# Kernel optimization log

Hardware: AMD Instinct MI355X
Metric: run time of the kernel (lower is better)

The kernel has to match this reference:

```python
import jax, jax.numpy as jnp
import numpy as np

EPS = 1e-07

def setup_inputs() -> dict:
    key = jax.random.key(0)
    foreground = jax.random.normal(key, (8, 256, 64, 64), dtype=jnp.float32)
    return {"foreground": foreground}

def reference(foreground):
    bs, ch, h, w = foreground.shape
    # kernels: one 1x1 kernel per spatial position, L2-normalized over channels
    K = foreground.reshape(bs, ch, h * w).transpose(0, 2, 1) + EPS      # [b, hw, c]
    K = K / jnp.sqrt(jnp.sum(K * K, axis=2, keepdims=True))
    # conv2d with 1x1 kernels == per-pixel dot product against every kernel.
    # (padding=patch_size//2 in the torch code is exactly cancelled by the
    #  matching padding of the conv_transpose2d, so it is omitted.)
    scores = jnp.einsum('bkc,bchw->bkhw', K, foreground)                # [b, hw, h, w]
    attn = jax.nn.softmax(scores, axis=1)
    # conv_transpose2d with the same 1x1 kernels == K^T @ attn per pixel
    out = jnp.einsum('bkc,bkhw->bchw', K, attn)                         # [b, c, h, w]
    return out
```

## Files before the change

kernel.cpp:

```cpp
#include <hip/hip_runtime.h>


#define BATCH 8
#define CH 256
#define NPIX 4096
#define EPSV 1e-7f
#define L2E 1.4426950408889634f

using bf16x8 = __attribute__((ext_vector_type(8))) __bf16;
using bf16x4 = __attribute__((ext_vector_type(4))) __bf16;
using f32x4  = __attribute__((ext_vector_type(4))) float;

__device__ __forceinline__ void gload16(const void* g, void* l) {
  __builtin_amdgcn_global_load_lds(
      (const __attribute__((address_space(1))) unsigned int*)g,
      (__attribute__((address_space(3))) unsigned int*)l, 16, 0, 0);
}

__device__ __forceinline__ void barrier_full() {
  asm volatile("s_waitcnt vmcnt(0) lgkmcnt(0)\n"
               "s_barrier" ::: "memory");
}
__device__ __forceinline__ void barrier_lgkm() {
  asm volatile("s_waitcnt lgkmcnt(0)\n"
               "s_barrier" ::: "memory");
}

__global__ __launch_bounds__(256)
void ca_prep(const float* __restrict__ F, __bf16* __restrict__ KA,
             __bf16* __restrict__ KB) {
  const int b   = blockIdx.x;
  const int kt  = blockIdx.y;
  const int kt0 = kt * 32;
  const int t   = threadIdx.x;
  const int k   = t & 31;
  const int h   = (t >> 5) & 1;
  const int w   = t >> 6;

  const float* __restrict__ Fb = F + (size_t)b * CH * NPIX;

  __shared__ float red[4][32];
  __shared__ float invk[32];
  __shared__ __align__(16) __bf16 T[32][264];

  float fv[32];
  float ss = 0.f;
#pragma unroll
  for (int rep = 0; rep < 32; ++rep) {
    int c = rep * 8 + w * 2 + h;
    float v = Fb[(size_t)c * NPIX + kt0 + k] + EPSV;
    fv[rep] = v;
    ss = fmaf(v, v, ss);
  }
  ss += __shfl_xor(ss, 32, 64);
  if ((t & 32) == 0) red[w][k] = ss;
  __syncthreads();
  if (t < 32) invk[t] = rsqrtf(red[0][t] + red[1][t] + red[2][t] + red[3][t]);
  __syncthreads();
  const float iv = invk[k];
#pragma unroll
  for (int rep = 0; rep < 32; ++rep) {
    int c = rep * 8 + w * 2 + h;
    T[k][c] = (__bf16)(fv[rep] * iv);
  }
  __syncthreads();

  __bf16* KAp = KA + ((size_t)b * 128 + kt) * (32 * 256);
#pragma unroll
  for (int pass = 0; pass < 4; ++pass) {
    int kk = pass * 8 + (t >> 5);
    int u  = t & 31;
    bf16x8 v = *(const bf16x8*)&T[kk][u * 8];
    *(bf16x8*)&KAp[kk * 256 + ((u ^ (kk & 7)) * 8)] = v;
  }
  __bf16* KBp = KB + ((size_t)b * 128 + kt) * (256 * 32);
#pragma unroll
  for (int pass = 0; pass < 4; ++pass) {
    int c = pass * 64 + (t >> 2);
    int v = t & 3;
    bf16x8 o;
#pragma unroll
    for (int j = 0; j < 8; ++j) o[j] = T[v * 8 + j][c];
    *(bf16x8*)&KBp[c * 32 + v * 8] = o;
  }
}

__global__ __launch_bounds__(1024, 4)
void ca_attn9(const float* __restrict__ F, const __bf16* __restrict__ KA,
              const __bf16* __restrict__ KB, float* __restrict__ Out) {
  __shared__ __align__(16) char smem[98304];

  const int tid  = threadIdx.x;
  const int lane = tid & 63;
  const int w    = tid >> 6;
  const int lq   = lane & 15;
  const int lg   = lane >> 4;
  const int b    = blockIdx.x;
  const int q0   = blockIdx.y * 128;

  const char* KAb = (const char*)(KA + (size_t)b * (size_t)NPIX * CH);
  const char* KBb = (const char*)(KB + (size_t)b * (size_t)NPIX * CH);
  char* PlB = smem + 65536;

  if (w < 8) {
    const int kh = w >> 2, qh = w & 3;
    const int qA = q0 + qh * 32 + lq;
    const int qB = qA + 16;
    const float* __restrict__ Fb = F + (size_t)b * CH * NPIX;
    const int wo = w * 4096;

#pragma unroll
    for (int j = 0; j < 4; ++j)
      gload16(KAb + wo + j * 1024 + lane * 16, smem + wo + j * 1024);

    bf16x8 qfA[8], qfB[8];
    float ssA = 0.f, ssB = 0.f;
#pragma unroll
    for (int cf = 0; cf < 8; ++cf) {
#pragma unroll
      for (int j = 0; j < 8; ++j) {
        int c = cf * 32 + lg * 8 + j;
        float va = Fb[(size_t)c * NPIX + qA];
        float vb = Fb[(size_t)c * NPIX + qB];
        qfA[cf][j] = (__bf16)(va * L2E);
        qfB[cf][j] = (__bf16)(vb * L2E);
        ssA = fmaf(va, va, ssA);
        ssB = fmaf(vb, vb, ssB);
      }
    }
    ssA += __shfl_xor(ssA, 16, 64); ssA += __shfl_xor(ssA, 32, 64);
    ssB += __shfl_xor(ssB, 16, 64); ssB += __shfl_xor(ssB, 32, 64);
    const float mqA = sqrtf(ssA) * L2E, mqB = sqrtf(ssB) * L2E;

    float lA = 0.f, lB = 0.f;
    const int krow = kh * 16 + lq;
    const int ksw  = lq & 7;
    const int rowByte = krow * 512;
    const int pwRowA = (qh * 32 + lq) * 128;
    const int pwRowB = pwRowA + 16 * 128;
    const int puBase = kh * 2 + (lg >> 1);
    const int pwSub  = ((lg & 1) << 3);
    const int u0 = (puBase ^ ksw) << 4;
    const int u1 = ((4 + puBase) ^ ksw) << 4;

    barrier_full();

    const f32x4 zero = {0.f, 0.f, 0.f, 0.f};
    for (int i = 0; i < 64; ++i) {
      const int cb = i & 1;
      if (i < 63) {
        const char* s = KAb + (size_t)(i + 1) * 32768;
        char* d = smem + (cb ^ 1) * 32768;
#pragma unroll
        for (int j = 0; j < 4; ++j)
          gload16(s + wo + j * 1024 + lane * 16, d + wo + j * 1024);
      }

      const char* ab0 = smem + cb * 32768 + rowByte;
      const char* ab1 = ab0 + 16384;
      f32x4 s00 = zero, s01 = zero, s10 = zero, s11 = zero;
      __builtin_amdgcn_s_setprio(1);
#pragma unroll
      for (int cf = 0; cf < 8; ++cf) {
        const int uo = ((((cf << 2) | lg) ^ ksw) << 4);
        bf16x8 a0 = *(const bf16x8*)(ab0 + uo);
        bf16x8 a1 = *(const bf16x8*)(ab1 + uo);
        s00 = __builtin_amdgcn_mfma_f32_16x16x32_bf16(a0, qfA[cf], s00, 0, 0, 0);
        s01 = __builtin_amdgcn_mfma_f32_16x16x32_bf16(a0, qfB[cf], s01, 0, 0, 0);
        s10 = __builtin_amdgcn_mfma_f32_16x16x32_bf16(a1, qfA[cf], s10, 0, 0, 0);
        s11 = __builtin_amdgcn_mfma_f32_16x16x32_bf16(a1, qfB[cf], s11, 0, 0, 0);
      }
      __builtin_amdgcn_s_setprio(0);

      char* pb = PlB + cb * 16384;
      bf16x4 pv00, pv01, pv10, pv11;
#pragma unroll
      for (int r = 0; r < 4; ++r) {
        float p00 = __builtin_amdgcn_exp2f(s00[r] - mqA);
        float p01 = __builtin_amdgcn_exp2f(s01[r] - mqB);
        float p10 = __builtin_amdgcn_exp2f(s10[r] - mqA);
        float p11 = __builtin_amdgcn_exp2f(s11[r] - mqB);
        lA += p00 + p10; lB += p01 + p11;
        pv00[r] = (__bf16)p00; pv01[r] = (__bf16)p01;
        pv10[r] = (__bf16)p10; pv11[r] = (__bf16)p11;
      }
      *(bf16x4*)(pb + pwRowA + u0 + pwSub) = pv00;
      *(bf16x4*)(pb + pwRowB + u0 + pwSub) = pv01;
      *(bf16x4*)(pb + pwRowA + u1 + pwSub) = pv10;
      *(bf16x4*)(pb + pwRowB + u1 + pwSub) = pv11;

      barrier_full();
    }

    lA += __shfl_xor(lA, 16, 64); lA += __shfl_xor(lA, 32, 64);
    lB += __shfl_xor(lB, 16, 64); lB += __shfl_xor(lB, 32, 64);
    float* lE = (float*)smem;
    if (lg == 0) lE[kh * 128 + qh * 32 + lq] = lA;
    if (lg == 1) lE[kh * 128 + qh * 32 + 16 + lq] = lB;
    barrier_full();

  } else {
    const int cq  = w - 8;
    const int c0  = (cq >> 1) * 64;
    const int qh2 = cq & 1;
    const size_t fragBase = (size_t)(c0 + lq) * 64 + (size_t)lg * 16;
    const int prRow = (qh2 * 64 + lq) * 128;
    const int prU0  = ((0 * 4 + lg) ^ (lq & 7)) << 4;
    const int prU1  = ((1 * 4 + lg) ^ (lq & 7)) << 4;

    const f32x4 zero = {0.f, 0.f, 0.f, 0.f};
    f32x4 oacc[4][4];
#pragma unroll
    for (int i = 0; i < 4; ++i)
#pragma unroll
      for (int j = 0; j < 4; ++j) oacc[i][j] = zero;

    barrier_lgkm();

    for (int jt = 0; jt < 64; ++jt) {
      const char* kb0 = KBb + (size_t)(2 * jt) * 16384 + fragBase;
      const char* kb1 = kb0 + 16384;
      bf16x8 k00 = *(const bf16x8*)(kb0);
      bf16x8 k01 = *(const bf16x8*)(kb0 + 1024);
      bf16x8 k02 = *(const bf16x8*)(kb0 + 2048);
      bf16x8 k03 = *(const bf16x8*)(kb0 + 3072);
      bf16x8 k10 = *(const bf16x8*)(kb1);
      bf16x8 k11 = *(const bf16x8*)(kb1 + 1024);
      bf16x8 k12 = *(const bf16x8*)(kb1 + 2048);
      bf16x8 k13 = *(const bf16x8*)(kb1 + 3072);

      barrier_lgkm();

      const char* pb = PlB + (jt & 1) * 16384;
      __builtin_amdgcn_s_setprio(1);
#pragma unroll
      for (int qf = 0; qf < 4; ++qf) {
        bf16x8 pf0 = *(const bf16x8*)(pb + prRow + qf * 2048 + prU0);
        oacc[0][qf] = __builtin_amdgcn_mfma_f32_16x16x32_bf16(k00, pf0, oacc[0][qf], 0, 0, 0);
        oacc[1][qf] = __builtin_amdgcn_mfma_f32_16x16x32_bf16(k01, pf0, oacc[1][qf], 0, 0, 0);
        oacc[2][qf] = __builtin_amdgcn_mfma_f32_16x16x32_bf16(k02, pf0, oacc[2][qf], 0, 0, 0);
        oacc[3][qf] = __builtin_amdgcn_mfma_f32_16x16x32_bf16(k03, pf0, oacc[3][qf], 0, 0, 0);
      }
#pragma unroll
      for (int qf = 0; qf < 4; ++qf) {
        bf16x8 pf1 = *(const bf16x8*)(pb + prRow + qf * 2048 + prU1);
        oacc[0][qf] = __builtin_amdgcn_mfma_f32_16x16x32_bf16(k10, pf1, oacc[0][qf], 0, 0, 0);
        oacc[1][qf] = __builtin_amdgcn_mfma_f32_16x16x32_bf16(k11, pf1, oacc[1][qf], 0, 0, 0);
        oacc[2][qf] = __builtin_amdgcn_mfma_f32_16x16x32_bf16(k12, pf1, oacc[2][qf], 0, 0, 0);
        oacc[3][qf] = __builtin_amdgcn_mfma_f32_16x16x32_bf16(k13, pf1, oacc[3][qf], 0, 0, 0);
      }
      __builtin_amdgcn_s_setprio(0);
    }

    barrier_lgkm();

    const float* lE = (const float*)smem;
    const int qb = qh2 * 64;
    float rl0 = 1.0f / (lE[qb + 0 * 16 + lq] + lE[128 + qb + 0 * 16 + lq]);
    float rl1 = 1.0f / (lE[qb + 1 * 16 + lq] + lE[128 + qb + 1 * 16 + lq]);
    float rl2 = 1.0f / (lE[qb + 2 * 16 + lq] + lE[128 + qb + 2 * 16 + lq]);
    float rl3 = 1.0f / (lE[qb + 3 * 16 + lq] + lE[128 + qb + 3 * 16 + lq]);
    float* __restrict__ Ob = Out + (size_t)b * CH * NPIX;
#pragma unroll
    for (int ct = 0; ct < 4; ++ct) {
#pragma unroll
      for (int r = 0; r < 4; ++r) {
        const int c = c0 + ct * 16 + lg * 4 + r;
        float* orow = Ob + (size_t)c * NPIX + q0 + qb;
        orow[0 * 16 + lq] = oacc[ct][0][r] * rl0;
        orow[1 * 16 + lq] = oacc[ct][1][r] * rl1;
        orow[2 * 16 + lq] = oacc[ct][2][r] * rl2;
        orow[3 * 16 + lq] = oacc[ct][3][r] * rl3;
      }
    }
  }
}

extern "C" void kernel_launch(void* const* d_in, const int* in_sizes, int n_in,
                              void* d_out, int out_size, void* d_ws, size_t ws_size,
                              hipStream_t stream) {
  const float* F = (const float*)d_in[0];
  float* out = (float*)d_out;
  const size_t imgElems = (size_t)BATCH * NPIX * CH;

  __bf16* KAi = (__bf16*)d_ws;
  __bf16* KBi = KAi + imgElems;
  ca_prep<<<dim3(BATCH, 128), 256, 0, stream>>>(F, KAi, KBi);
  ca_attn9<<<dim3(BATCH, 32), 1024, 0, stream>>>(F, KAi, KBi, out);
}
```

Before: 133.1 us.

## Switch PV consumer waves to 32x32x16 MFMA with matching KB layout

The consumer waves that accumulate K^T·P now use 32x32x16 bf16 MFMAs on 32x32 output tiles instead of 16x16x32 MFMAs on 16x16 tiles. The prep kernel writes KB in a new chunked layout so each lane's operand fragment is one contiguous 16-byte load. This cuts the number of MFMA issues and P-fragment LDS reads per iteration. The producer waves also keep raised priority through the softmax and P store, which may favour them over the consumer waves.

```diff
diff --git a/kernel.cpp b/kernel.cpp
--- a/kernel.cpp
+++ b/kernel.cpp
@@ -10,6 +10,7 @@
 using bf16x8 = __attribute__((ext_vector_type(8))) __bf16;
 using bf16x4 = __attribute__((ext_vector_type(4))) __bf16;
 using f32x4  = __attribute__((ext_vector_type(4))) float;
+using f32x16 = __attribute__((ext_vector_type(16))) float;
 
 __device__ __forceinline__ void gload16(const void* g, void* l) {
   __builtin_amdgcn_global_load_lds(
@@ -73,21 +74,26 @@
     bf16x8 v = *(const bf16x8*)&T[kk][u * 8];
     *(bf16x8*)&KAp[kk * 256 + ((u ^ (kk & 7)) * 8)] = v;
   }
-  __bf16* KBp = KB + ((size_t)b * 128 + kt) * (256 * 32);
-#pragma unroll
-  for (int pass = 0; pass < 4; ++pass) {
-    int c = pass * 64 + (t >> 2);
-    int v = t & 3;
-    bf16x8 o;
-#pragma unroll
-    for (int j = 0; j < 8; ++j) o[j] = T[v * 8 + j][c];
-    *(bf16x8*)&KBp[c * 32 + v * 8] = o;
+  {
+    const int jt = kt >> 1;
+    char* KBp = (char*)KB + ((size_t)b * 64 + jt) * 32768;
+#pragma unroll
+    for (int pass = 0; pass < 4; ++pass) {
+      int c  = pass * 64 + (t >> 2);
+      int v  = t & 3;
+      int kc = (kt & 1) * 2 + (v >> 1);
+      int hi = v & 1;
+      bf16x8 o;
+#pragma unroll
+      for (int j = 0; j < 8; ++j) o[j] = T[v * 8 + j][c];
+      *(bf16x8*)(KBp + kc * 8192 + c * 32 + hi * 16) = o;
+    }
   }
 }
 
 __global__ __launch_bounds__(1024, 4)
-void ca_attn9(const float* __restrict__ F, const __bf16* __restrict__ KA,
-              const __bf16* __restrict__ KB, float* __restrict__ Out) {
+void ca_attn10(const float* __restrict__ F, const __bf16* __restrict__ KA,
+               const __bf16* __restrict__ KB, float* __restrict__ Out) {
   __shared__ __align__(16) char smem[98304];
 
   const int tid  = threadIdx.x;
@@ -156,10 +162,11 @@
           gload16(s + wo + j * 1024 + lane * 16, d + wo + j * 1024);
       }
 
+      __builtin_amdgcn_s_setprio(1);
+
       const char* ab0 = smem + cb * 32768 + rowByte;
       const char* ab1 = ab0 + 16384;
       f32x4 s00 = zero, s01 = zero, s10 = zero, s11 = zero;
-      __builtin_amdgcn_s_setprio(1);
 #pragma unroll
       for (int cf = 0; cf < 8; ++cf) {
         const int uo = ((((cf << 2) | lg) ^ ksw) << 4);
@@ -170,7 +177,6 @@
         s10 = __builtin_amdgcn_mfma_f32_16x16x32_bf16(a1, qfA[cf], s10, 0, 0, 0);
         s11 = __builtin_amdgcn_mfma_f32_16x16x32_bf16(a1, qfB[cf], s11, 0, 0, 0);
       }
-      __builtin_amdgcn_s_setprio(0);
 
       char* pb = PlB + cb * 16384;
       bf16x4 pv00, pv01, pv10, pv11;
@@ -188,6 +194,7 @@
       *(bf16x4*)(pb + pwRowB + u0 + pwSub) = pv01;
       *(bf16x4*)(pb + pwRowA + u1 + pwSub) = pv10;
       *(bf16x4*)(pb + pwRowB + u1 + pwSub) = pv11;
+      __builtin_amdgcn_s_setprio(0);
 
       barrier_full();
     }
@@ -203,75 +210,62 @@
     const int cq  = w - 8;
     const int c0  = (cq >> 1) * 64;
     const int qh2 = cq & 1;
-    const size_t fragBase = (size_t)(c0 + lq) * 64 + (size_t)lg * 16;
-    const int prRow = (qh2 * 64 + lq) * 128;
-    const int prU0  = ((0 * 4 + lg) ^ (lq & 7)) << 4;
-    const int prU1  = ((1 * 4 + lg) ^ (lq & 7)) << 4;
-
-    const f32x4 zero = {0.f, 0.f, 0.f, 0.f};
-    f32x4 oacc[4][4];
-#pragma unroll
-    for (int i = 0; i < 4; ++i)
-#pragma unroll
-      for (int j = 0; j < 4; ++j) oacc[i][j] = zero;
+    const int l31 = lane & 31;
+    const int hi  = lane >> 5;
+    const size_t cBase = (size_t)(c0 + l31) * 32 + (size_t)hi * 16;
+    const int q7 = l31 & 7;
+    const int prRow0 = (qh2 * 64 + l31) * 128;
+    const int prRow1 = prRow0 + 32 * 128;
+
+    f32x16 o00 = (f32x16)0.0f, o01 = (f32x16)0.0f;
+    f32x16 o10 = (f32x16)0.0f, o11 = (f32x16)0.0f;
 
     barrier_lgkm();
 
     for (int jt = 0; jt < 64; ++jt) {
-      const char* kb0 = KBb + (size_t)(2 * jt) * 16384 + fragBase;
-      const char* kb1 = kb0 + 16384;
-      bf16x8 k00 = *(const bf16x8*)(kb0);
-      bf16x8 k01 = *(const bf16x8*)(kb0 + 1024);
-      bf16x8 k02 = *(const bf16x8*)(kb0 + 2048);
-      bf16x8 k03 = *(const bf16x8*)(kb0 + 3072);
-      bf16x8 k10 = *(const bf16x8*)(kb1);
-      bf16x8 k11 = *(const bf16x8*)(kb1 + 1024);
-      bf16x8 k12 = *(const bf16x8*)(kb1 + 2048);
-      bf16x8 k13 = *(const bf16x8*)(kb1 + 3072);
+      const char* kcb = KBb + (size_t)jt * 32768;
+      bf16x8 a00 = *(const bf16x8*)(kcb + 0 * 8192 + cBase);
+      bf16x8 a01 = *(const bf16x8*)(kcb + 1 * 8192 + cBase);
+      bf16x8 a02 = *(const bf16x8*)(kcb + 2 * 8192 + cBase);
+      bf16x8 a03 = *(const bf16x8*)(kcb + 3 * 8192 + cBase);
+      bf16x8 a10 = *(const bf16x8*)(kcb + 0 * 8192 + cBase + 1024);
+      bf16x8 a11 = *(const bf16x8*)(kcb + 1 * 8192 + cBase + 1024);
+      bf16x8 a12 = *(const bf16x8*)(kcb + 2 * 8192 + cBase + 1024);
+      bf16x8 a13 = *(const bf16x8*)(kcb + 3 * 8192 + cBase + 1024);
 
       barrier_lgkm();
 
       const char* pb = PlB + (jt & 1) * 16384;
-      __builtin_amdgcn_s_setprio(1);
-#pragma unroll
-      for (int qf = 0; qf < 4; ++qf) {
-        bf16x8 pf0 = *(const bf16x8*)(pb + prRow + qf * 2048 + prU0);
-        oacc[0][qf] = __builtin_amdgcn_mfma_f32_16x16x32_bf16(k00, pf0, oacc[0][qf], 0, 0, 0);
-        oacc[1][qf] = __builtin_amdgcn_mfma_f32_16x16x32_bf16(k01, pf0, oacc[1][qf], 0, 0, 0);
-        oacc[2][qf] = __builtin_amdgcn_mfma_f32_16x16x32_bf16(k02, pf0, oacc[2][qf], 0, 0, 0);
-        oacc[3][qf] = __builtin_amdgcn_mfma_f32_16x16x32_bf16(k03, pf0, oacc[3][qf], 0, 0, 0);
-      }
-#pragma unroll
-      for (int qf = 0; qf < 4; ++qf) {
-        bf16x8 pf1 = *(const bf16x8*)(pb + prRow + qf * 2048 + prU1);
-        oacc[0][qf] = __builtin_amdgcn_mfma_f32_16x16x32_bf16(k10, pf1, oacc[0][qf], 0, 0, 0);
-        oacc[1][qf] = __builtin_amdgcn_mfma_f32_16x16x32_bf16(k11, pf1, oacc[1][qf], 0, 0, 0);
-        oacc[2][qf] = __builtin_amdgcn_mfma_f32_16x16x32_bf16(k12, pf1, oacc[2][qf], 0, 0, 0);
-        oacc[3][qf] = __builtin_amdgcn_mfma_f32_16x16x32_bf16(k13, pf1, oacc[3][qf], 0, 0, 0);
-      }
-      __builtin_amdgcn_s_setprio(0);
+#pragma unroll
+      for (int kc = 0; kc < 4; ++kc) {
+        const int uo = (((kc << 1) | hi) ^ q7) << 4;
+        bf16x8 p0 = *(const bf16x8*)(pb + prRow0 + uo);
+        bf16x8 p1 = *(const bf16x8*)(pb + prRow1 + uo);
+        bf16x8 a0 = kc == 0 ? a00 : kc == 1 ? a01 : kc == 2 ? a02 : a03;
+        bf16x8 a1 = kc == 0 ? a10 : kc == 1 ? a11 : kc == 2 ? a12 : a13;
+        o00 = __builtin_amdgcn_mfma_f32_32x32x16_bf16(a0, p0, o00, 0, 0, 0);
+        o01 = __builtin_amdgcn_mfma_f32_32x32x16_bf16(a0, p1, o01, 0, 0, 0);
+        o10 = __builtin_amdgcn_mfma_f32_32x32x16_bf16(a1, p0, o10, 0, 0, 0);
+        o11 = __builtin_amdgcn_mfma_f32_32x32x16_bf16(a1, p1, o11, 0, 0, 0);
+      }
     }
 
     barrier_lgkm();
 
     const float* lE = (const float*)smem;
     const int qb = qh2 * 64;
-    float rl0 = 1.0f / (lE[qb + 0 * 16 + lq] + lE[128 + qb + 0 * 16 + lq]);
-    float rl1 = 1.0f / (lE[qb + 1 * 16 + lq] + lE[128 + qb + 1 * 16 + lq]);
-    float rl2 = 1.0f / (lE[qb + 2 * 16 + lq] + lE[128 + qb + 2 * 16 + lq]);
-    float rl3 = 1.0f / (lE[qb + 3 * 16 + lq] + lE[128 + qb + 3 * 16 + lq]);
+    const float rl0 = 1.0f / (lE[qb + l31] + lE[128 + qb + l31]);
+    const float rl1 = 1.0f / (lE[qb + 32 + l31] + lE[128 + qb + 32 + l31]);
     float* __restrict__ Ob = Out + (size_t)b * CH * NPIX;
 #pragma unroll
-    for (int ct = 0; ct < 4; ++ct) {
-#pragma unroll
-      for (int r = 0; r < 4; ++r) {
-        const int c = c0 + ct * 16 + lg * 4 + r;
-        float* orow = Ob + (size_t)c * NPIX + q0 + qb;
-        orow[0 * 16 + lq] = oacc[ct][0][r] * rl0;
-        orow[1 * 16 + lq] = oacc[ct][1][r] * rl1;
-        orow[2 * 16 + lq] = oacc[ct][2][r] * rl2;
-        orow[3 * 16 + lq] = oacc[ct][3][r] * rl3;
-      }
+    for (int r = 0; r < 16; ++r) {
+      const int crow = (r & 3) + 8 * (r >> 2) + 4 * hi;
+      float* orow0 = Ob + (size_t)(c0 + crow) * NPIX + q0 + qb;
+      float* orow1 = Ob + (size_t)(c0 + 32 + crow) * NPIX + q0 + qb;
+      orow0[l31]      = o00[r] * rl0;
+      orow0[32 + l31] = o01[r] * rl1;
+      orow1[l31]      = o10[r] * rl0;
+      orow1[32 + l31] = o11[r] * rl1;
     }
   }
 }
@@ -286,5 +280,5 @@
   __bf16* KAi = (__bf16*)d_ws;
   __bf16* KBi = KAi + imgElems;
   ca_prep<<<dim3(BATCH, 128), 256, 0, stream>>>(F, KAi, KBi);
-  ca_attn9<<<dim3(BATCH, 32), 1024, 0, stream>>>(F, KAi, KBi, out);
-}
+  ca_attn10<<<dim3(BATCH, 32), 1024, 0, stream>>>(F, KAi, KBi, out);
+}
```

New measurement: 139.6 us. 4.9% more time.

## Store key tiles in MFMA fragment order and load them directly from global

Applied to the files above, without the earlier changes.

The prep kernel now writes the normalized key matrix in a fragment-ordered layout, so each lane's 16-byte MFMA operand sits at a contiguous, coalesced address. The score-producing waves then read key fragments straight from global/L2 into registers, replacing the double-buffered global_load_lds staging through a 64 KB LDS region. This cuts LDS use to the probability buffers, which may allow more blocks per CU, and removes the vmcnt waits from the barriers. In exchange, the score MFMAs depend on global-load latency inside the loop, with no explicit prefetch to hide it.

```diff
diff --git a/kernel.cpp b/kernel.cpp
--- a/kernel.cpp
+++ b/kernel.cpp
@@ -11,23 +11,13 @@
 using bf16x4 = __attribute__((ext_vector_type(4))) __bf16;
 using f32x4  = __attribute__((ext_vector_type(4))) float;
 
-__device__ __forceinline__ void gload16(const void* g, void* l) {
-  __builtin_amdgcn_global_load_lds(
-      (const __attribute__((address_space(1))) unsigned int*)g,
-      (__attribute__((address_space(3))) unsigned int*)l, 16, 0, 0);
-}
-
-__device__ __forceinline__ void barrier_full() {
-  asm volatile("s_waitcnt vmcnt(0) lgkmcnt(0)\n"
-               "s_barrier" ::: "memory");
-}
 __device__ __forceinline__ void barrier_lgkm() {
   asm volatile("s_waitcnt lgkmcnt(0)\n"
                "s_barrier" ::: "memory");
 }
 
 __global__ __launch_bounds__(256)
-void ca_prep(const float* __restrict__ F, __bf16* __restrict__ KA,
+void ca_prep(const float* __restrict__ F, __bf16* __restrict__ KAF,
              __bf16* __restrict__ KB) {
   const int b   = blockIdx.x;
   const int kt  = blockIdx.y;
@@ -65,30 +55,38 @@
   }
   __syncthreads();
 
-  __bf16* KAp = KA + ((size_t)b * 128 + kt) * (32 * 256);
-#pragma unroll
-  for (int pass = 0; pass < 4; ++pass) {
-    int kk = pass * 8 + (t >> 5);
-    int u  = t & 31;
-    bf16x8 v = *(const bf16x8*)&T[kk][u * 8];
-    *(bf16x8*)&KAp[kk * 256 + ((u ^ (kk & 7)) * 8)] = v;
-  }
-  __bf16* KBp = KB + ((size_t)b * 128 + kt) * (256 * 32);
-#pragma unroll
-  for (int pass = 0; pass < 4; ++pass) {
-    int c = pass * 64 + (t >> 2);
-    int v = t & 3;
-    bf16x8 o;
-#pragma unroll
-    for (int j = 0; j < 8; ++j) o[j] = T[v * 8 + j][c];
-    *(bf16x8*)&KBp[c * 32 + v * 8] = o;
+  {
+    const int jt = kt >> 1, st = kt & 1;
+    char* KAFp = (char*)KAF + ((size_t)b * 64 + jt) * 32768 + st * 16384;
+#pragma unroll
+    for (int pass = 0; pass < 4; ++pass) {
+      int slot = pass * 256 + t;
+      int cf   = slot >> 7;
+      int krow = (slot >> 2) & 31;
+      int lgi  = slot & 3;
+      bf16x8 v = *(const bf16x8*)&T[krow][cf * 32 + lgi * 8];
+      *(bf16x8*)(KAFp + slot * 16) = v;
+    }
+  }
+  {
+    __bf16* KBp = KB + ((size_t)b * 128 + kt) * (256 * 32);
+#pragma unroll
+    for (int pass = 0; pass < 4; ++pass) {
+      int c = pass * 64 + (t >> 2);
+      int v = t & 3;
+      bf16x8 o;
+#pragma unroll
+      for (int j = 0; j < 8; ++j) o[j] = T[v * 8 + j][c];
+      *(bf16x8*)&KBp[c * 32 + v * 8] = o;
+    }
   }
 }
 
 __global__ __launch_bounds__(1024, 4)
-void ca_attn9(const float* __restrict__ F, const __bf16* __restrict__ KA,
-              const __bf16* __restrict__ KB, float* __restrict__ Out) {
-  __shared__ __align__(16) char smem[98304];
+void ca_attn11(const float* __restrict__ F, const __bf16* __restrict__ KAF,
+               const __bf16* __restrict__ KB, float* __restrict__ Out) {
+  __shared__ __align__(16) char Pl[2][16384];
+  __shared__ float lE[256];
 
   const int tid  = threadIdx.x;
   const int lane = tid & 63;
@@ -98,20 +96,14 @@
   const int b    = blockIdx.x;
   const int q0   = blockIdx.y * 128;
 
-  const char* KAb = (const char*)(KA + (size_t)b * (size_t)NPIX * CH);
-  const char* KBb = (const char*)(KB + (size_t)b * (size_t)NPIX * CH);
-  char* PlB = smem + 65536;
+  const char* KFb = (const char*)KAF + (size_t)b * (size_t)NPIX * CH * 2;
+  const char* KBb = (const char*)KB + (size_t)b * (size_t)NPIX * CH * 2;
 
   if (w < 8) {
     const int kh = w >> 2, qh = w & 3;
     const int qA = q0 + qh * 32 + lq;
     const int qB = qA + 16;
     const float* __restrict__ Fb = F + (size_t)b * CH * NPIX;
-    const int wo = w * 4096;
-
-#pragma unroll
-    for (int j = 0; j < 4; ++j)
-      gload16(KAb + wo + j * 1024 + lane * 16, smem + wo + j * 1024);
 
     bf16x8 qfA[8], qfB[8];
     float ssA = 0.f, ssB = 0.f;
@@ -133,9 +125,8 @@
     const float mqA = sqrtf(ssA) * L2E, mqB = sqrtf(ssB) * L2E;
 
     float lA = 0.f, lB = 0.f;
-    const int krow = kh * 16 + lq;
-    const int ksw  = lq & 7;
-    const int rowByte = krow * 512;
+    const int ksw = lq & 7;
+    const char* abase0 = KFb + kh * 1024 + lq * 64 + lg * 16;
     const int pwRowA = (qh * 32 + lq) * 128;
     const int pwRowB = pwRowA + 16 * 128;
     const int puBase = kh * 2 + (lg >> 1);
@@ -143,28 +134,19 @@
     const int u0 = (puBase ^ ksw) << 4;
     const int u1 = ((4 + puBase) ^ ksw) << 4;
 
-    barrier_full();
+    barrier_lgkm();
 
     const f32x4 zero = {0.f, 0.f, 0.f, 0.f};
     for (int i = 0; i < 64; ++i) {
       const int cb = i & 1;
-      if (i < 63) {
-        const char* s = KAb + (size_t)(i + 1) * 32768;
-        char* d = smem + (cb ^ 1) * 32768;
-#pragma unroll
-        for (int j = 0; j < 4; ++j)
-          gload16(s + wo + j * 1024 + lane * 16, d + wo + j * 1024);
-      }
-
-      const char* ab0 = smem + cb * 32768 + rowByte;
-      const char* ab1 = ab0 + 16384;
+      const char* ab = abase0 + (size_t)i * 32768;
+
       f32x4 s00 = zero, s01 = zero, s10 = zero, s11 = zero;
       __builtin_amdgcn_s_setprio(1);
 #pragma unroll
       for (int cf = 0; cf < 8; ++cf) {
-        const int uo = ((((cf << 2) | lg) ^ ksw) << 4);
-        bf16x8 a0 = *(const bf16x8*)(ab0 + uo);
-        bf16x8 a1 = *(const bf16x8*)(ab1 + uo);
+        bf16x8 a0 = *(const bf16x8*)(ab + cf * 2048);
+        bf16x8 a1 = *(const bf16x8*)(ab + 16384 + cf * 2048);
         s00 = __builtin_amdgcn_mfma_f32_16x16x32_bf16(a0, qfA[cf], s00, 0, 0, 0);
         s01 = __builtin_amdgcn_mfma_f32_16x16x32_bf16(a0, qfB[cf], s01, 0, 0, 0);
         s10 = __builtin_amdgcn_mfma_f32_16x16x32_bf16(a1, qfA[cf], s10, 0, 0, 0);
@@ -172,7 +154,7 @@
       }
       __builtin_amdgcn_s_setprio(0);
 
-      char* pb = PlB + cb * 16384;
+      char* pb = Pl[cb];
       bf16x4 pv00, pv01, pv10, pv11;
 #pragma unroll
       for (int r = 0; r < 4; ++r) {
@@ -189,15 +171,14 @@
       *(bf16x4*)(pb + pwRowA + u1 + pwSub) = pv10;
       *(bf16x4*)(pb + pwRowB + u1 + pwSub) = pv11;
 
-      barrier_full();
+      barrier_lgkm();
     }
 
     lA += __shfl_xor(lA, 16, 64); lA += __shfl_xor(lA, 32, 64);
     lB += __shfl_xor(lB, 16, 64); lB += __shfl_xor(lB, 32, 64);
-    float* lE = (float*)smem;
     if (lg == 0) lE[kh * 128 + qh * 32 + lq] = lA;
     if (lg == 1) lE[kh * 128 + qh * 32 + 16 + lq] = lB;
-    barrier_full();
+    barrier_lgkm();
 
   } else {
     const int cq  = w - 8;
@@ -231,7 +212,7 @@
 
       barrier_lgkm();
 
-      const char* pb = PlB + (jt & 1) * 16384;
+      const char* pb = Pl[jt & 1];
       __builtin_amdgcn_s_setprio(1);
 #pragma unroll
       for (int qf = 0; qf < 4; ++qf) {
@@ -254,7 +235,6 @@
 
     barrier_lgkm();
 
-    const float* lE = (const float*)smem;
     const int qb = qh2 * 64;
     float rl0 = 1.0f / (lE[qb + 0 * 16 + lq] + lE[128 + qb + 0 * 16 + lq]);
     float rl1 = 1.0f / (lE[qb + 1 * 16 + lq] + lE[128 + qb + 1 * 16 + lq]);
@@ -283,8 +263,8 @@
   float* out = (float*)d_out;
   const size_t imgElems = (size_t)BATCH * NPIX * CH;
 
-  __bf16* KAi = (__bf16*)d_ws;
-  __bf16* KBi = KAi + imgElems;
-  ca_prep<<<dim3(BATCH, 128), 256, 0, stream>>>(F, KAi, KBi);
-  ca_attn9<<<dim3(BATCH, 32), 1024, 0, stream>>>(F, KAi, KBi, out);
-}
+  __bf16* KAFi = (__bf16*)d_ws;
+  __bf16* KBi  = KAFi + imgElems;
+  ca_prep<<<dim3(BATCH, 128), 256, 0, stream>>>(F, KAFi, KBi);
+  ca_attn11<<<dim3(BATCH, 32), 1024, 0, stream>>>(F, KAFi, KBi, out);
+}
```

After: 240.6 us. +80.8%, slower.

## Use fp8 e4m3 MFMA for the score GEMM instead of bf16

Applied to the files above, without the earlier changes.

Normalized kernels (KA) and the log2e-scaled queries are now quantized to fp8 e4m3, and the QK score MFMAs use the 16x16x32 fp8 instruction. This halves the KA tile bytes streamed from global memory into LDS, shrinks shared memory from 96KB to 64KB, and adjusts the swizzle for 8-byte fragments. The cost is reduced score precision before the exponential, which could raise output error; the PV half stays bf16.

```diff
diff --git a/kernel.cpp b/kernel.cpp
--- a/kernel.cpp
+++ b/kernel.cpp
@@ -1,4 +1,5 @@
 #include <hip/hip_runtime.h>
+#include <hip/hip_fp8.h>
 
 
 #define BATCH 8
@@ -26,8 +27,12 @@
                "s_barrier" ::: "memory");
 }
 
+__device__ __forceinline__ unsigned char to_fp8(float f) {
+  return __hip_cvt_float_to_fp8(f, __HIP_SATFINITE, __HIP_E4M3);
+}
+
 __global__ __launch_bounds__(256)
-void ca_prep(const float* __restrict__ F, __bf16* __restrict__ KA,
+void ca_prep(const float* __restrict__ F, unsigned char* __restrict__ KA,
              __bf16* __restrict__ KB) {
   const int b   = blockIdx.x;
   const int kt  = blockIdx.y;
@@ -65,30 +70,38 @@
   }
   __syncthreads();
 
-  __bf16* KAp = KA + ((size_t)b * 128 + kt) * (32 * 256);
-#pragma unroll
-  for (int pass = 0; pass < 4; ++pass) {
-    int kk = pass * 8 + (t >> 5);
-    int u  = t & 31;
-    bf16x8 v = *(const bf16x8*)&T[kk][u * 8];
-    *(bf16x8*)&KAp[kk * 256 + ((u ^ (kk & 7)) * 8)] = v;
-  }
-  __bf16* KBp = KB + ((size_t)b * 128 + kt) * (256 * 32);
-#pragma unroll
-  for (int pass = 0; pass < 4; ++pass) {
-    int c = pass * 64 + (t >> 2);
-    int v = t & 3;
-    bf16x8 o;
-#pragma unroll
-    for (int j = 0; j < 8; ++j) o[j] = T[v * 8 + j][c];
-    *(bf16x8*)&KBp[c * 32 + v * 8] = o;
+  {
+    char* KAp = (char*)KA + ((size_t)b * 128 + kt) * (32 * 256);
+#pragma unroll
+    for (int pass = 0; pass < 4; ++pass) {
+      int slot = pass * 256 + t;
+      int krow = slot >> 5;
+      int u    = slot & 31;
+      bf16x8 v = *(const bf16x8*)&T[krow][u * 8];
+      unsigned char pk[8];
+#pragma unroll
+      for (int j = 0; j < 8; ++j) pk[j] = to_fp8((float)v[j]);
+      *(long*)(KAp + krow * 256 + ((u ^ (krow & 15)) * 8)) = *(const long*)pk;
+    }
+  }
+  {
+    __bf16* KBp = KB + ((size_t)b * 128 + kt) * (256 * 32);
+#pragma unroll
+    for (int pass = 0; pass < 4; ++pass) {
+      int c = pass * 64 + (t >> 2);
+      int v = t & 3;
+      bf16x8 o;
+#pragma unroll
+      for (int j = 0; j < 8; ++j) o[j] = T[v * 8 + j][c];
+      *(bf16x8*)&KBp[c * 32 + v * 8] = o;
+    }
   }
 }
 
 __global__ __launch_bounds__(1024, 4)
-void ca_attn9(const float* __restrict__ F, const __bf16* __restrict__ KA,
-              const __bf16* __restrict__ KB, float* __restrict__ Out) {
-  __shared__ __align__(16) char smem[98304];
+void ca_attn12(const float* __restrict__ F, const unsigned char* __restrict__ KA,
+               const __bf16* __restrict__ KB, float* __restrict__ Out) {
+  __shared__ __align__(16) char smem[65536];
 
   const int tid  = threadIdx.x;
   const int lane = tid & 63;
@@ -98,35 +111,38 @@
   const int b    = blockIdx.x;
   const int q0   = blockIdx.y * 128;
 
-  const char* KAb = (const char*)(KA + (size_t)b * (size_t)NPIX * CH);
-  const char* KBb = (const char*)(KB + (size_t)b * (size_t)NPIX * CH);
-  char* PlB = smem + 65536;
+  const char* KAb = (const char*)KA + (size_t)b * (size_t)NPIX * CH;
+  const char* KBb = (const char*)KB + (size_t)b * (size_t)NPIX * CH * 2;
+  char* PlB = smem + 32768;
 
   if (w < 8) {
     const int kh = w >> 2, qh = w & 3;
     const int qA = q0 + qh * 32 + lq;
     const int qB = qA + 16;
     const float* __restrict__ Fb = F + (size_t)b * CH * NPIX;
-    const int wo = w * 4096;
-
-#pragma unroll
-    for (int j = 0; j < 4; ++j)
+    const int wo = w * 2048;
+
+#pragma unroll
+    for (int j = 0; j < 2; ++j)
       gload16(KAb + wo + j * 1024 + lane * 16, smem + wo + j * 1024);
 
-    bf16x8 qfA[8], qfB[8];
+    long qpA[8], qpB[8];
     float ssA = 0.f, ssB = 0.f;
 #pragma unroll
     for (int cf = 0; cf < 8; ++cf) {
+      unsigned char pa[8], pb8[8];
 #pragma unroll
       for (int j = 0; j < 8; ++j) {
         int c = cf * 32 + lg * 8 + j;
         float va = Fb[(size_t)c * NPIX + qA];
         float vb = Fb[(size_t)c * NPIX + qB];
-        qfA[cf][j] = (__bf16)(va * L2E);
-        qfB[cf][j] = (__bf16)(vb * L2E);
+        pa[j]  = to_fp8(va * L2E);
+        pb8[j] = to_fp8(vb * L2E);
         ssA = fmaf(va, va, ssA);
         ssB = fmaf(vb, vb, ssB);
       }
+      qpA[cf] = *(const long*)pa;
+      qpB[cf] = *(const long*)pb8;
     }
     ssA += __shfl_xor(ssA, 16, 64); ssA += __shfl_xor(ssA, 32, 64);
     ssB += __shfl_xor(ssB, 16, 64); ssB += __shfl_xor(ssB, 32, 64);
@@ -134,8 +150,8 @@
 
     float lA = 0.f, lB = 0.f;
     const int krow = kh * 16 + lq;
-    const int ksw  = lq & 7;
-    const int rowByte = krow * 512;
+    const int rowByte = krow * 256;
+    const int ksw = lq & 7;
     const int pwRowA = (qh * 32 + lq) * 128;
     const int pwRowB = pwRowA + 16 * 128;
     const int puBase = kh * 2 + (lg >> 1);
@@ -149,26 +165,26 @@
     for (int i = 0; i < 64; ++i) {
       const int cb = i & 1;
       if (i < 63) {
-        const char* s = KAb + (size_t)(i + 1) * 32768;
-        char* d = smem + (cb ^ 1) * 32768;
-#pragma unroll
-        for (int j = 0; j < 4; ++j)
+        const char* s = KAb + (size_t)(i + 1) * 16384;
+        char* d = smem + (cb ^ 1) * 16384;
+#pragma unroll
+        for (int j = 0; j < 2; ++j)
           gload16(s + wo + j * 1024 + lane * 16, d + wo + j * 1024);
       }
 
-      const char* ab0 = smem + cb * 32768 + rowByte;
-      const char* ab1 = ab0 + 16384;
+      const char* ab0 = smem + cb * 16384 + rowByte;
+      const char* ab1 = ab0 + 8192;
       f32x4 s00 = zero, s01 = zero, s10 = zero, s11 = zero;
       __builtin_amdgcn_s_setprio(1);
 #pragma unroll
       for (int cf = 0; cf < 8; ++cf) {
-        const int uo = ((((cf << 2) | lg) ^ ksw) << 4);
-        bf16x8 a0 = *(const bf16x8*)(ab0 + uo);
-        bf16x8 a1 = *(const bf16x8*)(ab1 + uo);
-        s00 = __builtin_amdgcn_mfma_f32_16x16x32_bf16(a0, qfA[cf], s00, 0, 0, 0);
-        s01 = __builtin_amdgcn_mfma_f32_16x16x32_bf16(a0, qfB[cf], s01, 0, 0, 0);
-        s10 = __builtin_amdgcn_mfma_f32_16x16x32_bf16(a1, qfA[cf], s10, 0, 0, 0);
-        s11 = __builtin_amdgcn_mfma_f32_16x16x32_bf16(a1, qfB[cf], s11, 0, 0, 0);
+        const int uo = ((((cf << 2) | lg) ^ lq) << 3);
+        long a0 = *(const long*)(ab0 + uo);
+        long a1 = *(const long*)(ab1 + uo);
+        s00 = __builtin_amdgcn_mfma_f32_16x16x32_fp8_fp8(a0, qpA[cf], s00, 0, 0, 0);
+        s01 = __builtin_amdgcn_mfma_f32_16x16x32_fp8_fp8(a0, qpB[cf], s01, 0, 0, 0);
+        s10 = __builtin_amdgcn_mfma_f32_16x16x32_fp8_fp8(a1, qpA[cf], s10, 0, 0, 0);
+        s11 = __builtin_amdgcn_mfma_f32_16x16x32_fp8_fp8(a1, qpB[cf], s11, 0, 0, 0);
       }
       __builtin_amdgcn_s_setprio(0);
 
@@ -281,10 +297,10 @@
                               hipStream_t stream) {
   const float* F = (const float*)d_in[0];
   float* out = (float*)d_out;
-  const size_t imgElems = (size_t)BATCH * NPIX * CH;
-
-  __bf16* KAi = (__bf16*)d_ws;
-  __bf16* KBi = KAi + imgElems;
+  const size_t imgBytes = (size_t)BATCH * NPIX * CH;
+
+  unsigned char* KAi = (unsigned char*)d_ws;
+  __bf16* KBi = (__bf16*)((char*)d_ws + imgBytes);
   ca_prep<<<dim3(BATCH, 128), 256, 0, stream>>>(F, KAi, KBi);
-  ca_attn9<<<dim3(BATCH, 32), 1024, 0, stream>>>(F, KAi, KBi, out);
-}
+  ca_attn12<<<dim3(BATCH, 32), 1024, 0, stream>>>(F, KAi, KBi, out);
+}
```

New measurement: 127.7 us. -4.1%, faster.
